# Optimization experiments

Hardware: AMD Instinct MI355X
Metric: run time of the kernel (lower is better)

The kernel has to match this reference:

```python
import jax, jax.numpy as jnp
import numpy as np
from jax import lax

H = 128; NOISE = 128; L = 16; A = 10; HYB = 3; F_NODE = 17; E_FEAT = 4
TEMP = 1.0
MAX_VALENCES = jnp.array([4., 3., 2., 1., 4., 2., 6., 1., 4., 4.], dtype=jnp.float32)


def setup_inputs():
    key = jax.random.key(0)
    ks = jax.random.split(key, 16)
    B, N = 4096, 32
    def w(k, *s):
        return jax.random.normal(k, s, dtype=jnp.float32) * 0.05
    return {
        'noise': jax.random.normal(ks[0], (B, NOISE), dtype=jnp.float32),
        'w1': w(ks[1], NOISE, H), 'b1': jnp.zeros((H,), jnp.float32),
        'gat_w': w(ks[2], L, H, H), 'gat_b': jnp.zeros((L, H), jnp.float32),
        'att_src': w(ks[3], L, H), 'att_dst': w(ks[4], L, H),
        'w_atom': w(ks[5], H, A), 'b_atom': jnp.zeros((A,), jnp.float32),
        'w_hyb': w(ks[6], H, HYB), 'b_hyb': jnp.zeros((HYB,), jnp.float32),
        'w_deg': w(ks[7], H, 1), 'b_deg': jnp.zeros((1,), jnp.float32),
        'w_chg': w(ks[8], H, 1), 'b_chg': jnp.zeros((1,), jnp.float32),
        'w_arom': w(ks[9], H, 1), 'b_arom': jnp.zeros((1,), jnp.float32),
        'w_eex': w(ks[10], 2 * F_NODE, 1), 'b_eex': jnp.zeros((1,), jnp.float32),
        'w_ety': w(ks[11], 2 * F_NODE, E_FEAT), 'b_ety': jnp.zeros((E_FEAT,), jnp.float32),
        'batch_size': B, 'num_nodes': N,
    }


def _gumbel(k, shape):
    u = jax.random.uniform(k, shape, minval=1e-6, maxval=1.0 - 1e-6)
    return -jnp.log(-jnp.log(u))


def reference(noise, w1, b1, gat_w, gat_b, att_src, att_dst, w_atom, b_atom,
              w_hyb, b_hyb, w_deg, b_deg, w_chg, b_chg, w_arom, b_arom,
              w_eex, b_eex, w_ety, b_ety, batch_size, num_nodes):
    B, N = batch_size, num_nodes
    h0 = jax.nn.relu(noise @ w1 + b1)                      # [B,H]
    x = jnp.broadcast_to(h0[:, None, :], (B, N, h0.shape[-1]))
    idx = jnp.arange(N)
    # chain adjacency (both directions) + self loops (PyG GATConv default)
    adj = (jnp.abs(idx[:, None] - idx[None, :]) == 1) | (idx[:, None] == idx[None, :])
    neg = jnp.float32(-1e9)

    def layer(xc, p):
        W, b, a_s, a_d = p
        h = xc @ W + b                                     # [B,N,H]
        e_src = h @ a_s                                    # [B,N]
        e_dst = h @ a_d
        s = jax.nn.leaky_relu(e_dst[:, :, None] + e_src[:, None, :], 0.2)  # [B,N,N]
        s = jnp.where(adj, s, neg)
        alpha = jax.nn.softmax(s, axis=-1)
        out = jnp.einsum('bij,bjh->bih', alpha, h)
        return jax.nn.relu(out + xc), None                 # residual GAT layer

    x, _ = lax.scan(layer, x, (gat_w, gat_b, att_src, att_dst))

    sk = jax.random.split(jax.random.key(42), 4)
    # atom type head + categorical sampling (Gumbel-max on logits/T)
    atom_logits = x @ w_atom + b_atom                      # [B,N,A]
    atom_lp = jax.nn.log_softmax(atom_logits, axis=-1)
    atom_idx = jnp.argmax(atom_logits / TEMP + _gumbel(sk[0], atom_logits.shape), axis=-1)
    atom_lp_mol = jnp.take_along_axis(atom_lp, atom_idx[..., None], axis=-1)[..., 0].mean(axis=1)
    # hybridization head
    hyb_logits = x @ w_hyb + b_hyb                         # [B,N,3]
    hyb_lp = jax.nn.log_softmax(hyb_logits, axis=-1)
    hyb_idx = jnp.argmax(hyb_logits / TEMP + _gumbel(sk[1], hyb_logits.shape), axis=-1)
    hyb_lp_mol = jnp.take_along_axis(hyb_lp, hyb_idx[..., None], axis=-1)[..., 0].mean(axis=1)
    # remaining node heads
    deg = jax.nn.sigmoid(x @ w_deg + b_deg)
    chg = jnp.tanh(lax.stop_gradient(x @ w_chg + b_chg))   # .clone().detach() in torch
    arom_p = jax.nn.sigmoid(x @ w_arom + b_arom)
    arom = (jax.random.uniform(sk[2], arom_p.shape) < arom_p).astype(jnp.float32)
    val = (MAX_VALENCES[atom_idx] / 5.0)[..., None]
    node_features = jnp.concatenate([
        jax.nn.one_hot(atom_idx, A, dtype=jnp.float32), deg, chg,
        jax.nn.one_hot(hyb_idx, HYB, dtype=jnp.float32), arom, val], axis=-1)  # [B,N,17]
    # edge heads on chain edges (both directions)
    u = jnp.arange(N - 1); v = u + 1
    eu = jnp.concatenate([u, v]); ev = jnp.concatenate([v, u])
    ef = jnp.concatenate([node_features[:, eu], node_features[:, ev]], axis=-1)  # [B,2(N-1),34]
    exist_p = jax.nn.sigmoid(ef @ w_eex + b_eex)[..., 0]
    edge_mask = exist_p > 0.5
    type_logits = ef @ w_ety + b_ety
    type_idx = jnp.argmax(type_logits / TEMP + _gumbel(sk[3], type_logits.shape), axis=-1)
    edge_attr = jax.nn.one_hot(type_idx, E_FEAT, dtype=jnp.float32)
    return node_features, atom_lp_mol, hyb_lp_mol, edge_attr, edge_mask
```

## Files before the change

### kernel.cpp

```cpp
#include <hip/hip_runtime.h>
#include <stdint.h>
#include <math.h>


struct U2 { uint32_t a, b; };

__device__ __forceinline__ U2 threefry(uint32_t k0, uint32_t k1, uint32_t x0, uint32_t x1) {
  const uint32_t ks2 = k0 ^ k1 ^ 0x1BD11BDAu;
#define TFR(r) { x0 += x1; x1 = (x1 << (r)) | (x1 >> (32 - (r))); x1 ^= x0; }
  x0 += k0;  x1 += k1;
  TFR(13) TFR(15) TFR(26) TFR(6)
  x0 += k1;  x1 += ks2 + 1u;
  TFR(17) TFR(29) TFR(16) TFR(24)
  x0 += ks2; x1 += k0 + 2u;
  TFR(13) TFR(15) TFR(26) TFR(6)
  x0 += k0;  x1 += k1 + 3u;
  TFR(17) TFR(29) TFR(16) TFR(24)
  x0 += k1;  x1 += ks2 + 4u;
  TFR(13) TFR(15) TFR(26) TFR(6)
  x0 += ks2; x1 += k0 + 5u;
#undef TFR
  U2 r; r.a = x0; r.b = x1; return r;
}

__device__ __forceinline__ uint32_t pbits(uint32_t k0, uint32_t k1, uint32_t ctr) {
  U2 r = threefry(k0, k1, 0u, ctr);
  return r.a ^ r.b;
}

__device__ __forceinline__ float bits_to_unit(uint32_t bits) {
  return __uint_as_float((bits >> 9) | 0x3f800000u) - 1.0f;
}

__device__ __forceinline__ float jgumbel(uint32_t k0, uint32_t k1, uint32_t ctr) {
  const float minv = 1e-6f;
  const float maxv = (float)(1.0 - 1e-6);
  const float span = maxv - minv;
  float f = bits_to_unit(pbits(k0, k1, ctr));
  float u = fmaxf(minv, __fadd_rn(__fmul_rn(f, span), minv));
  return -logf(-logf(u));
}

extern "C" __global__ void __launch_bounds__(256)
gen_kernel(const float* __restrict__ noise,
           const float* __restrict__ w1,
           const float* __restrict__ b1,
           const float* __restrict__ gat_w,
           const float* __restrict__ gat_b,
           const float* __restrict__ w_atom,
           const float* __restrict__ b_atom,
           const float* __restrict__ w_hyb,
           const float* __restrict__ b_hyb,
           const float* __restrict__ w_deg,
           const float* __restrict__ b_deg,
           const float* __restrict__ w_chg,
           const float* __restrict__ b_chg,
           const float* __restrict__ w_arom,
           const float* __restrict__ b_arom,
           const float* __restrict__ w_eex,
           const float* __restrict__ b_eex,
           const float* __restrict__ w_ety,
           const float* __restrict__ b_ety,
           float* __restrict__ out)
{
  __shared__ __align__(16) double sXa[4][128][2];
  __shared__ __align__(16) double sXb[4][128][2];
  __shared__ double sScr[4][4][16];
  __shared__ float  sNF[4][4][32][17];
  __shared__ double sLP[4][4][64];

  const int t       = threadIdx.x;
  const int wv      = t >> 6;
  const int ln      = t & 63;
  const int molBase = blockIdx.x * 16 + wv * 4;
  const int c0      = ln << 1;

  {
    const float2 n0 = *(const float2*)(noise + (size_t)(molBase + 0) * 128 + c0);
    const float2 n1 = *(const float2*)(noise + (size_t)(molBase + 1) * 128 + c0);
    const float2 n2 = *(const float2*)(noise + (size_t)(molBase + 2) * 128 + c0);
    const float2 n3 = *(const float2*)(noise + (size_t)(molBase + 3) * 128 + c0);
    double2 v;
    v.x = (double)n0.x; v.y = (double)n1.x; *(double2*)&sXa[wv][c0][0]     = v;
    v.x = (double)n2.x; v.y = (double)n3.x; *(double2*)&sXb[wv][c0][0]     = v;
    v.x = (double)n0.y; v.y = (double)n1.y; *(double2*)&sXa[wv][c0 + 1][0] = v;
    v.x = (double)n2.y; v.y = (double)n3.y; *(double2*)&sXb[wv][c0 + 1][0] = v;
  }

  double2 xr0, xr1, xr2, xr3;

  #pragma unroll 1
  for (int l = 0; l < 17; ++l) {
    const float* __restrict__ W  = (l == 0) ? w1 : (gat_w + (((size_t)(l - 1)) << 14));
    const float* __restrict__ bp = (l == 0) ? b1 : (gat_b + ((l - 1) << 7));

    double a0x = 0.0, a0y = 0.0, a1x = 0.0, a1y = 0.0;
    double a2x = 0.0, a2y = 0.0, a3x = 0.0, a3y = 0.0;

    float2  wA[8];  double2 xaA[8], xbA[8];
    float2  wB[8];  double2 xaB[8], xbB[8];

    #pragma unroll
    for (int j = 0; j < 8; ++j) {
      wA[j]  = *(const float2*)(W + (j << 7) + c0);
      xaA[j] = *(const double2*)&sXa[wv][j][0];
      xbA[j] = *(const double2*)&sXb[wv][j][0];
    }

    #pragma unroll
    for (int ch = 0; ch < 16; ++ch) {
      const int nb = (ch + 1) << 3;
      if ((ch & 1) == 0) {
        if (ch < 15) {
          #pragma unroll
          for (int j = 0; j < 8; ++j) {
            wB[j]  = *(const float2*)(W + ((nb + j) << 7) + c0);
            xaB[j] = *(const double2*)&sXa[wv][nb + j][0];
            xbB[j] = *(const double2*)&sXb[wv][nb + j][0];
          }
        }
        #pragma unroll
        for (int j = 0; j < 8; ++j) {
          const double wx = (double)wA[j].x, wy = (double)wA[j].y;
          a0x = fma(xaA[j].x, wx, a0x); a0y = fma(xaA[j].x, wy, a0y);
          a1x = fma(xaA[j].y, wx, a1x); a1y = fma(xaA[j].y, wy, a1y);
          a2x = fma(xbA[j].x, wx, a2x); a2y = fma(xbA[j].x, wy, a2y);
          a3x = fma(xbA[j].y, wx, a3x); a3y = fma(xbA[j].y, wy, a3y);
        }
      } else {
        if (ch < 15) {
          #pragma unroll
          for (int j = 0; j < 8; ++j) {
            wA[j]  = *(const float2*)(W + ((nb + j) << 7) + c0);
            xaA[j] = *(const double2*)&sXa[wv][nb + j][0];
            xbA[j] = *(const double2*)&sXb[wv][nb + j][0];
          }
        }
        #pragma unroll
        for (int j = 0; j < 8; ++j) {
          const double wx = (double)wB[j].x, wy = (double)wB[j].y;
          a0x = fma(xaB[j].x, wx, a0x); a0y = fma(xaB[j].x, wy, a0y);
          a1x = fma(xaB[j].y, wx, a1x); a1y = fma(xaB[j].y, wy, a1y);
          a2x = fma(xbB[j].x, wx, a2x); a2y = fma(xbB[j].x, wy, a2y);
          a3x = fma(xbB[j].y, wx, a3x); a3y = fma(xbB[j].y, wy, a3y);
        }
      }
    }

    const float2 bb = *(const float2*)(bp + c0);
    const double bx = (double)bb.x, by = (double)bb.y;
    if (l == 0) {
      xr0.x = fmax(a0x + bx, 0.0); xr0.y = fmax(a0y + by, 0.0);
      xr1.x = fmax(a1x + bx, 0.0); xr1.y = fmax(a1y + by, 0.0);
      xr2.x = fmax(a2x + bx, 0.0); xr2.y = fmax(a2y + by, 0.0);
      xr3.x = fmax(a3x + bx, 0.0); xr3.y = fmax(a3y + by, 0.0);
    } else {
      xr0.x = fmax(xr0.x + a0x + bx, 0.0); xr0.y = fmax(xr0.y + a0y + by, 0.0);
      xr1.x = fmax(xr1.x + a1x + bx, 0.0); xr1.y = fmax(xr1.y + a1y + by, 0.0);
      xr2.x = fmax(xr2.x + a2x + bx, 0.0); xr2.y = fmax(xr2.y + a2y + by, 0.0);
      xr3.x = fmax(xr3.x + a3x + bx, 0.0); xr3.y = fmax(xr3.y + a3y + by, 0.0);
    }
    double2 v;
    v.x = xr0.x; v.y = xr1.x; *(double2*)&sXa[wv][c0][0]     = v;
    v.x = xr2.x; v.y = xr3.x; *(double2*)&sXb[wv][c0][0]     = v;
    v.x = xr0.y; v.y = xr1.y; *(double2*)&sXa[wv][c0 + 1][0] = v;
    v.x = xr2.y; v.y = xr3.y; *(double2*)&sXb[wv][c0 + 1][0] = v;
  }

  {
    const int mloc = ln >> 4;
    const int h    = ln & 15;
    const double* xsrc = (mloc < 2) ? &sXa[wv][0][mloc] : &sXb[wv][0][mloc - 2];
    const float* wp; int stride; double bias;
    if (h < 10)       { wp = w_atom + h;        stride = 10; bias = (double)b_atom[h]; }
    else if (h < 13)  { wp = w_hyb + (h - 10);  stride = 3;  bias = (double)b_hyb[h - 10]; }
    else if (h == 13) { wp = w_deg;             stride = 1;  bias = (double)b_deg[0]; }
    else if (h == 14) { wp = w_chg;             stride = 1;  bias = (double)b_chg[0]; }
    else              { wp = w_arom;            stride = 1;  bias = (double)b_arom[0]; }
    double acc = 0.0;
    for (int c = 0; c < 128; ++c)
      acc = fma(xsrc[(size_t)c * 2], (double)wp[c * stride], acc);
    sScr[wv][mloc][h] = acc + bias;
  }

  const U2 k0p = threefry(0u, 42u, 0u, 0u);
  const U2 k1p = threefry(0u, 42u, 0u, 1u);
  const U2 k2p = threefry(0u, 42u, 0u, 2u);
  const U2 k3p = threefry(0u, 42u, 0u, 3u);

  for (int r = 0; r < 2; ++r) {
    const int mloc = r * 2 + (ln >> 5);
    const int n    = ln & 31;
    const int mol  = molBase + mloc;
    const double* scr = sScr[wv][mloc];

    double m = scr[0];
    #pragma unroll
    for (int a = 1; a < 10; ++a) m = fmax(m, scr[a]);
    double lsum = 0.0;
    #pragma unroll
    for (int a = 0; a < 10; ++a) lsum += exp(scr[a] - m);
    const double lse = log(lsum);
    const uint32_t abase = ((uint32_t)mol * 32u + (uint32_t)n) * 10u;
    int asel = 0; double abest = 0.0;
    #pragma unroll
    for (int a = 0; a < 10; ++a) {
      const double g = (double)jgumbel(k0p.a, k0p.b, abase + (uint32_t)a);
      const double sc = scr[a] + g;
      if (a == 0 || sc > abest) { abest = sc; asel = a; }
    }
    sLP[wv][mloc][n] = (scr[asel] - m) - lse;

    double m2 = fmax(fmax(scr[10], scr[11]), scr[12]);
    double ls2 = exp(scr[10] - m2) + exp(scr[11] - m2) + exp(scr[12] - m2);
    const double lse2 = log(ls2);
    const uint32_t hbase = ((uint32_t)mol * 32u + (uint32_t)n) * 3u;
    int hsel = 0; double hbest = 0.0;
    #pragma unroll
    for (int j = 0; j < 3; ++j) {
      const double g = (double)jgumbel(k1p.a, k1p.b, hbase + (uint32_t)j);
      const double sc = scr[10 + j] + g;
      if (j == 0 || sc > hbest) { hbest = sc; hsel = j; }
    }
    sLP[wv][mloc][32 + n] = (scr[10 + hsel] - m2) - lse2;

    const double deg = 1.0 / (1.0 + exp(-scr[13]));
    const double chg = tanh(scr[14]);
    const double pr  = 1.0 / (1.0 + exp(-scr[15]));
    const uint32_t ridx = (uint32_t)mol * 32u + (uint32_t)n;
    const double uu = (double)bits_to_unit(pbits(k2p.a, k2p.b, ridx));
    const double arom = (uu < pr) ? 1.0 : 0.0;
    const double valt[10] = {4.0/5.0, 3.0/5.0, 2.0/5.0, 1.0/5.0, 4.0/5.0,
                             2.0/5.0, 6.0/5.0, 1.0/5.0, 4.0/5.0, 4.0/5.0};
    double nf[17];
    #pragma unroll
    for (int i = 0; i < 10; ++i) nf[i] = (i == asel) ? 1.0 : 0.0;
    nf[10] = deg; nf[11] = chg;
    #pragma unroll
    for (int j = 0; j < 3; ++j) nf[12 + j] = (j == hsel) ? 1.0 : 0.0;
    nf[15] = arom; nf[16] = valt[asel];

    const size_t o = ((size_t)mol * 32 + n) * 17;
    #pragma unroll
    for (int i = 0; i < 17; ++i) {
      sNF[wv][mloc][n][i] = (float)nf[i];
      out[o + i] = (float)nf[i];
    }
  }

  #pragma unroll 1
  for (int m = 0; m < 4; ++m) {
    const int mol = molBase + m;
    if (ln == 62) {
      double sa = 0.0;
      for (int n = 0; n < 32; ++n) sa += sLP[wv][m][n];
      out[2228224 + (size_t)mol] = (float)(sa / 32.0);
    } else if (ln == 63) {
      double sh = 0.0;
      for (int n = 0; n < 32; ++n) sh += sLP[wv][m][32 + n];
      out[2232320 + (size_t)mol] = (float)(sh / 32.0);
    } else {
      const int e = ln;
      const int nu_ = (e < 31) ? e : (e - 30);
      const int nv_ = (e < 31) ? (e + 1) : (e - 31);
      double lex = 0.0;
      double lt[4] = {0.0, 0.0, 0.0, 0.0};
      for (int i = 0; i < 17; ++i) {
        const double f = (double)sNF[wv][m][nu_][i];
        lex = fma(f, (double)w_eex[i], lex);
        #pragma unroll
        for (int c = 0; c < 4; ++c) lt[c] = fma(f, (double)w_ety[i * 4 + c], lt[c]);
      }
      for (int i = 0; i < 17; ++i) {
        const double f = (double)sNF[wv][m][nv_][i];
        lex = fma(f, (double)w_eex[17 + i], lex);
        #pragma unroll
        for (int c = 0; c < 4; ++c) lt[c] = fma(f, (double)w_ety[(17 + i) * 4 + c], lt[c]);
      }
      lex += (double)b_eex[0];
      #pragma unroll
      for (int c = 0; c < 4; ++c) lt[c] += (double)b_ety[c];

      const double pex = 1.0 / (1.0 + exp(-lex));
      out[3252224 + (size_t)mol * 62 + e] = (pex > 0.5) ? 1.f : 0.f;

      const uint32_t tbase = ((uint32_t)mol * 62u + (uint32_t)e) * 4u;
      int tsel = 0; double tbest = 0.0;
      #pragma unroll
      for (int c = 0; c < 4; ++c) {
        const double g = (double)jgumbel(k3p.a, k3p.b, tbase + (uint32_t)c);
        const double sc = lt[c] + g;
        if (c == 0 || sc > tbest) { tbest = sc; tsel = c; }
      }
      const size_t o = 2236416 + ((size_t)mol * 62 + e) * 4;
      #pragma unroll
      for (int c = 0; c < 4; ++c) out[o + c] = (c == tsel) ? 1.f : 0.f;
    }
  }
}

extern "C" void kernel_launch(void* const* d_in, const int* in_sizes, int n_in,
                              void* d_out, int out_size, void* d_ws, size_t ws_size,
                              hipStream_t stream) {
  (void)in_sizes; (void)n_in; (void)out_size; (void)d_ws; (void)ws_size;
  hipLaunchKernelGGL(gen_kernel, dim3(256), dim3(256), 0, stream,
                     (const float*)d_in[0],  (const float*)d_in[1],
                     (const float*)d_in[2],  (const float*)d_in[3],
                     (const float*)d_in[4],
                     (const float*)d_in[7],  (const float*)d_in[8],
                     (const float*)d_in[9],  (const float*)d_in[10],
                     (const float*)d_in[11], (const float*)d_in[12],
                     (const float*)d_in[13], (const float*)d_in[14],
                     (const float*)d_in[15], (const float*)d_in[16],
                     (const float*)d_in[17], (const float*)d_in[18],
                     (const float*)d_in[19], (const float*)d_in[20],
                     (float*)d_out);
}
```

Measured before the change: 203.4 us.

## Process two molecules per wavefront instead of four, doubling grid size

Each wavefront now owns two molecules instead of four, and the grid doubles from 256 to 512 blocks, so the work is spread across twice as many waves. The original 256 blocks of 4 waves underfill a GPU with 256 CUs; more waves improve latency hiding in the double-precision matmul chain. The trade-off is that each weight load from global or L2 is now reused across only 2 molecules instead of 4, doubling weight traffic, and fewer FMAs per load may expose more memory latency.

```diff
diff --git a/kernel.cpp b/kernel.cpp
--- a/kernel.cpp
+++ b/kernel.cpp
@@ -63,31 +63,26 @@
            const float* __restrict__ b_ety,
            float* __restrict__ out)
 {
-  __shared__ __align__(16) double sXa[4][128][2];
-  __shared__ __align__(16) double sXb[4][128][2];
-  __shared__ double sScr[4][4][16];
-  __shared__ float  sNF[4][4][32][17];
-  __shared__ double sLP[4][4][64];
+  __shared__ __align__(16) double sX[4][128][2];
+  __shared__ double sScr[4][2][16];
+  __shared__ float  sNF[4][2][32][17];
+  __shared__ double sLP[4][2][64];
 
   const int t       = threadIdx.x;
   const int wv      = t >> 6;
   const int ln      = t & 63;
-  const int molBase = blockIdx.x * 16 + wv * 4;
+  const int molPair = (blockIdx.x * 4 + wv) * 2;
   const int c0      = ln << 1;
 
   {
-    const float2 n0 = *(const float2*)(noise + (size_t)(molBase + 0) * 128 + c0);
-    const float2 n1 = *(const float2*)(noise + (size_t)(molBase + 1) * 128 + c0);
-    const float2 n2 = *(const float2*)(noise + (size_t)(molBase + 2) * 128 + c0);
-    const float2 n3 = *(const float2*)(noise + (size_t)(molBase + 3) * 128 + c0);
+    const float2 n0 = *(const float2*)(noise + (size_t)molPair * 128 + c0);
+    const float2 n1 = *(const float2*)(noise + (size_t)(molPair + 1) * 128 + c0);
     double2 v;
-    v.x = (double)n0.x; v.y = (double)n1.x; *(double2*)&sXa[wv][c0][0]     = v;
-    v.x = (double)n2.x; v.y = (double)n3.x; *(double2*)&sXb[wv][c0][0]     = v;
-    v.x = (double)n0.y; v.y = (double)n1.y; *(double2*)&sXa[wv][c0 + 1][0] = v;
-    v.x = (double)n2.y; v.y = (double)n3.y; *(double2*)&sXb[wv][c0 + 1][0] = v;
-  }
-
-  double2 xr0, xr1, xr2, xr3;
+    v.x = (double)n0.x; v.y = (double)n1.x; *(double2*)&sX[wv][c0][0]     = v;
+    v.x = (double)n0.y; v.y = (double)n1.y; *(double2*)&sX[wv][c0 + 1][0] = v;
+  }
+
+  double2 xr0, xr1;
 
   #pragma unroll 1
   for (int l = 0; l < 17; ++l) {
@@ -95,16 +90,14 @@
     const float* __restrict__ bp = (l == 0) ? b1 : (gat_b + ((l - 1) << 7));
 
     double a0x = 0.0, a0y = 0.0, a1x = 0.0, a1y = 0.0;
-    double a2x = 0.0, a2y = 0.0, a3x = 0.0, a3y = 0.0;
-
-    float2  wA[8];  double2 xaA[8], xbA[8];
-    float2  wB[8];  double2 xaB[8], xbB[8];
+
+    float2  wA[8];  double2 xA[8];
+    float2  wB[8];  double2 xB[8];
 
     #pragma unroll
     for (int j = 0; j < 8; ++j) {
-      wA[j]  = *(const float2*)(W + (j << 7) + c0);
-      xaA[j] = *(const double2*)&sXa[wv][j][0];
-      xbA[j] = *(const double2*)&sXb[wv][j][0];
+      wA[j] = *(const float2*)(W + (j << 7) + c0);
+      xA[j] = *(const double2*)&sX[wv][j][0];
     }
 
     #pragma unroll
@@ -114,35 +107,29 @@
         if (ch < 15) {
           #pragma unroll
           for (int j = 0; j < 8; ++j) {
-            wB[j]  = *(const float2*)(W + ((nb + j) << 7) + c0);
-            xaB[j] = *(const double2*)&sXa[wv][nb + j][0];
-            xbB[j] = *(const double2*)&sXb[wv][nb + j][0];
+            wB[j] = *(const float2*)(W + ((nb + j) << 7) + c0);
+            xB[j] = *(const double2*)&sX[wv][nb + j][0];
           }
         }
         #pragma unroll
         for (int j = 0; j < 8; ++j) {
           const double wx = (double)wA[j].x, wy = (double)wA[j].y;
-          a0x = fma(xaA[j].x, wx, a0x); a0y = fma(xaA[j].x, wy, a0y);
-          a1x = fma(xaA[j].y, wx, a1x); a1y = fma(xaA[j].y, wy, a1y);
-          a2x = fma(xbA[j].x, wx, a2x); a2y = fma(xbA[j].x, wy, a2y);
-          a3x = fma(xbA[j].y, wx, a3x); a3y = fma(xbA[j].y, wy, a3y);
+          a0x = fma(xA[j].x, wx, a0x); a0y = fma(xA[j].x, wy, a0y);
+          a1x = fma(xA[j].y, wx, a1x); a1y = fma(xA[j].y, wy, a1y);
         }
       } else {
         if (ch < 15) {
           #pragma unroll
           for (int j = 0; j < 8; ++j) {
-            wA[j]  = *(const float2*)(W + ((nb + j) << 7) + c0);
-            xaA[j] = *(const double2*)&sXa[wv][nb + j][0];
-            xbA[j] = *(const double2*)&sXb[wv][nb + j][0];
+            wA[j] = *(const float2*)(W + ((nb + j) << 7) + c0);
+            xA[j] = *(const double2*)&sX[wv][nb + j][0];
           }
         }
         #pragma unroll
         for (int j = 0; j < 8; ++j) {
           const double wx = (double)wB[j].x, wy = (double)wB[j].y;
-          a0x = fma(xaB[j].x, wx, a0x); a0y = fma(xaB[j].x, wy, a0y);
-          a1x = fma(xaB[j].y, wx, a1x); a1y = fma(xaB[j].y, wy, a1y);
-          a2x = fma(xbB[j].x, wx, a2x); a2y = fma(xbB[j].x, wy, a2y);
-          a3x = fma(xbB[j].y, wx, a3x); a3y = fma(xbB[j].y, wy, a3y);
+          a0x = fma(xB[j].x, wx, a0x); a0y = fma(xB[j].x, wy, a0y);
+          a1x = fma(xB[j].y, wx, a1x); a1y = fma(xB[j].y, wy, a1y);
         }
       }
     }
@@ -152,25 +139,19 @@
     if (l == 0) {
       xr0.x = fmax(a0x + bx, 0.0); xr0.y = fmax(a0y + by, 0.0);
       xr1.x = fmax(a1x + bx, 0.0); xr1.y = fmax(a1y + by, 0.0);
-      xr2.x = fmax(a2x + bx, 0.0); xr2.y = fmax(a2y + by, 0.0);
-      xr3.x = fmax(a3x + bx, 0.0); xr3.y = fmax(a3y + by, 0.0);
     } else {
       xr0.x = fmax(xr0.x + a0x + bx, 0.0); xr0.y = fmax(xr0.y + a0y + by, 0.0);
       xr1.x = fmax(xr1.x + a1x + bx, 0.0); xr1.y = fmax(xr1.y + a1y + by, 0.0);
-      xr2.x = fmax(xr2.x + a2x + bx, 0.0); xr2.y = fmax(xr2.y + a2y + by, 0.0);
-      xr3.x = fmax(xr3.x + a3x + bx, 0.0); xr3.y = fmax(xr3.y + a3y + by, 0.0);
     }
     double2 v;
-    v.x = xr0.x; v.y = xr1.x; *(double2*)&sXa[wv][c0][0]     = v;
-    v.x = xr2.x; v.y = xr3.x; *(double2*)&sXb[wv][c0][0]     = v;
-    v.x = xr0.y; v.y = xr1.y; *(double2*)&sXa[wv][c0 + 1][0] = v;
-    v.x = xr2.y; v.y = xr3.y; *(double2*)&sXb[wv][c0 + 1][0] = v;
-  }
-
-  {
-    const int mloc = ln >> 4;
-    const int h    = ln & 15;
-    const double* xsrc = (mloc < 2) ? &sXa[wv][0][mloc] : &sXb[wv][0][mloc - 2];
+    v.x = xr0.x; v.y = xr1.x; *(double2*)&sX[wv][c0][0]     = v;
+    v.x = xr0.y; v.y = xr1.y; *(double2*)&sX[wv][c0 + 1][0] = v;
+  }
+
+  if (ln < 32) {
+    const int mh = ln >> 4;
+    const int h  = ln & 15;
+    const double* xsrc = &sX[wv][0][mh];
     const float* wp; int stride; double bias;
     if (h < 10)       { wp = w_atom + h;        stride = 10; bias = (double)b_atom[h]; }
     else if (h < 13)  { wp = w_hyb + (h - 10);  stride = 3;  bias = (double)b_hyb[h - 10]; }
@@ -180,7 +161,7 @@
     double acc = 0.0;
     for (int c = 0; c < 128; ++c)
       acc = fma(xsrc[(size_t)c * 2], (double)wp[c * stride], acc);
-    sScr[wv][mloc][h] = acc + bias;
+    sScr[wv][mh][h] = acc + bias;
   }
 
   const U2 k0p = threefry(0u, 42u, 0u, 0u);
@@ -188,11 +169,11 @@
   const U2 k2p = threefry(0u, 42u, 0u, 2u);
   const U2 k3p = threefry(0u, 42u, 0u, 3u);
 
-  for (int r = 0; r < 2; ++r) {
-    const int mloc = r * 2 + (ln >> 5);
-    const int n    = ln & 31;
-    const int mol  = molBase + mloc;
-    const double* scr = sScr[wv][mloc];
+  {
+    const int mh  = ln >> 5;
+    const int n   = ln & 31;
+    const int mol = molPair + mh;
+    const double* scr = sScr[wv][mh];
 
     double m = scr[0];
     #pragma unroll
@@ -209,7 +190,7 @@
       const double sc = scr[a] + g;
       if (a == 0 || sc > abest) { abest = sc; asel = a; }
     }
-    sLP[wv][mloc][n] = (scr[asel] - m) - lse;
+    sLP[wv][mh][n] = (scr[asel] - m) - lse;
 
     double m2 = fmax(fmax(scr[10], scr[11]), scr[12]);
     double ls2 = exp(scr[10] - m2) + exp(scr[11] - m2) + exp(scr[12] - m2);
@@ -222,7 +203,7 @@
       const double sc = scr[10 + j] + g;
       if (j == 0 || sc > hbest) { hbest = sc; hsel = j; }
     }
-    sLP[wv][mloc][32 + n] = (scr[10 + hsel] - m2) - lse2;
+    sLP[wv][mh][32 + n] = (scr[10 + hsel] - m2) - lse2;
 
     const double deg = 1.0 / (1.0 + exp(-scr[13]));
     const double chg = tanh(scr[14]);
@@ -243,14 +224,14 @@
     const size_t o = ((size_t)mol * 32 + n) * 17;
     #pragma unroll
     for (int i = 0; i < 17; ++i) {
-      sNF[wv][mloc][n][i] = (float)nf[i];
+      sNF[wv][mh][n][i] = (float)nf[i];
       out[o + i] = (float)nf[i];
     }
   }
 
   #pragma unroll 1
-  for (int m = 0; m < 4; ++m) {
-    const int mol = molBase + m;
+  for (int m = 0; m < 2; ++m) {
+    const int mol = molPair + m;
     if (ln == 62) {
       double sa = 0.0;
       for (int n = 0; n < 32; ++n) sa += sLP[wv][m][n];
@@ -303,7 +284,7 @@
                               void* d_out, int out_size, void* d_ws, size_t ws_size,
                               hipStream_t stream) {
   (void)in_sizes; (void)n_in; (void)out_size; (void)d_ws; (void)ws_size;
-  hipLaunchKernelGGL(gen_kernel, dim3(256), dim3(256), 0, stream,
+  hipLaunchKernelGGL(gen_kernel, dim3(512), dim3(256), 0, stream,
                      (const float*)d_in[0],  (const float*)d_in[1],
                      (const float*)d_in[2],  (const float*)d_in[3],
                      (const float*)d_in[4],
```

After: 247.1 us. 21.5% more time.
